# Optimization experiments

Measured on AMD Instinct MI355X. Metric: run time of the kernel, lower is better.

The kernel has to match this reference:

```python
import jax, jax.numpy as jnp
import numpy as np

B, S, IN_DIM, OUT_DIM, HID = 16, 256, 128, 128, 512


def setup_inputs() -> dict:
    key = jax.random.key(0)
    ks = jax.random.split(key, 7)
    x = jax.random.normal(ks[0], (B, S, IN_DIM), dtype=jnp.float32)
    # hypernet linear 1: input_dim -> hyper_hidden_dim
    W1 = jax.random.normal(ks[1], (IN_DIM, HID), dtype=jnp.float32) / np.sqrt(IN_DIM)
    b1 = jax.random.normal(ks[2], (HID,), dtype=jnp.float32) * 0.01
    # hypernet linear 2: hyper_hidden_dim -> input_dim * output_dim
    W2 = jax.random.normal(ks[3], (HID, IN_DIM * OUT_DIM), dtype=jnp.float32) / np.sqrt(HID)
    b2 = jax.random.normal(ks[4], (IN_DIM * OUT_DIM,), dtype=jnp.float32) * 0.01
    # final fc: output_dim -> output_dim
    Wfc = jax.random.normal(ks[5], (OUT_DIM, OUT_DIM), dtype=jnp.float32) / np.sqrt(OUT_DIM)
    bfc = jax.random.normal(ks[6], (OUT_DIM,), dtype=jnp.float32) * 0.01
    return {"x": x, "W1": W1, "b1": b1, "W2": W2, "b2": b2, "Wfc": Wfc, "bfc": bfc}


def reference(x, W1, b1, W2, b2, Wfc, bfc):
    # hypernet: per-token generated weight matrix Wx [B,S,IN,OUT]
    h = jax.nn.relu(jnp.einsum('bsi,ih->bsh', x, W1) + b1)
    Wx = (jnp.einsum('bsh,ho->bso', h, W2) + b2).reshape(x.shape[0], x.shape[1], IN_DIM, OUT_DIM)
    # batched vector-matrix product per (b,s), then sum over s -> [B, OUT]
    y = jnp.einsum('bsi,bsio->bo', x, Wx)
    return y @ Wfc + bfc
```

## Files before the change

kernel.cpp:

```cpp
#include <hip/hip_runtime.h>


typedef __attribute__((ext_vector_type(8))) short     s16x8;
typedef __attribute__((ext_vector_type(8))) unsigned short u16x8;
typedef __attribute__((ext_vector_type(4))) float     f32x4;

__device__ __forceinline__ unsigned short f2bf(float f) {
    union { float f; unsigned int u; } v; v.f = f;
    unsigned int r = v.u + 0x7FFFu + ((v.u >> 16) & 1u);
    return (unsigned short)(r >> 16);
}
__device__ __forceinline__ float bf2f(unsigned short u) {
    union { unsigned int u; float f; } v; v.u = ((unsigned int)u) << 16;
    return v.f;
}

#define OFF_MP   0
#define OFF_PART 2097152
#define OFF_SXP  3145728

__global__ __launch_bounds__(256) void k_AB(const float* __restrict__ x,
        const float* __restrict__ W1, const float* __restrict__ b1,
        float* __restrict__ Mp, float* __restrict__ sxp) {
    __shared__ __align__(16) unsigned char smem[87296];
    auto Ws  = (unsigned short (*)[136])(smem);
    auto xA  = (unsigned short (*)[136])(smem + 17408);
    auto xTl = (unsigned short (*)[136])(smem + 52224);
    auto Wt  = (float (*)[33])(smem + 52224);
    float* b1s = (float*)(smem + 87040);
    auto hts = (unsigned short (*)[136])(smem);

    const int tid = threadIdx.x;
    const int b  = blockIdx.x >> 4;
    const int hb = (blockIdx.x >> 1) & 7;
    const int sh = blockIdx.x & 1;

    {
        const int r = tid >> 1, q = tid & 1;
        const float* xrow = &x[(size_t)(b * 256 + sh * 128 + r) * 128 + q * 64];
        #pragma unroll
        for (int m = 0; m < 8; ++m) {
            const float4 v0 = *(const float4*)&xrow[m * 8];
            const float4 v1 = *(const float4*)&xrow[m * 8 + 4];
            unsigned short t8[8] __attribute__((aligned(16))) = {
                f2bf(v0.x), f2bf(v0.y), f2bf(v0.z), f2bf(v0.w),
                f2bf(v1.x), f2bf(v1.y), f2bf(v1.z), f2bf(v1.w)};
            *(u16x8*)&xA[r][q * 64 + m * 8] = *(u16x8*)t8;
        }
        if (tid < 64) b1s[tid] = b1[hb * 64 + tid];
    }
    for (int hq = 0; hq < 2; ++hq) {
        __syncthreads();
        #pragma unroll
        for (int p = 0; p < 16; ++p) {
            const int flat = p * 256 + tid;
            const int i = flat >> 5, hc = flat & 31;
            Wt[i][hc] = W1[(size_t)i * 512 + hb * 64 + hq * 32 + hc];
        }
        __syncthreads();
        {
            const int h2 = tid >> 3, pt = tid & 7;
            unsigned short t16[16] __attribute__((aligned(16)));
            #pragma unroll
            for (int m = 0; m < 16; ++m)
                t16[m] = f2bf(Wt[pt * 16 + m][h2]);
            *(u16x8*)&Ws[hq * 32 + h2][pt * 16]     = *(u16x8*)&t16[0];
            *(u16x8*)&Ws[hq * 32 + h2][pt * 16 + 8] = *(u16x8*)&t16[8];
        }
    }
    __syncthreads();

    const int w = tid >> 6, lane = tid & 63;
    const int wr = w >> 1, wc = w & 1;
    const int l15 = lane & 15, kl = lane >> 4;
    f32x4 zero = {0.f, 0.f, 0.f, 0.f};

    f32x4 acc[4][2];
    #pragma unroll
    for (int i = 0; i < 4; ++i)
        #pragma unroll
        for (int j = 0; j < 2; ++j) acc[i][j] = zero;
    #pragma unroll
    for (int ks = 0; ks < 4; ++ks) {
        s16x8 a[4], bb[2];
        #pragma unroll
        for (int f = 0; f < 4; ++f)
            a[f] = *(const s16x8*)&xA[wr * 64 + f * 16 + l15][ks * 32 + kl * 8];
        #pragma unroll
        for (int f = 0; f < 2; ++f)
            bb[f] = *(const s16x8*)&Ws[wc * 32 + f * 16 + l15][ks * 32 + kl * 8];
        #pragma unroll
        for (int fr = 0; fr < 4; ++fr)
            #pragma unroll
            for (int fc = 0; fc < 2; ++fc)
                acc[fr][fc] = __builtin_amdgcn_mfma_f32_16x16x32_bf16(a[fr], bb[fc], acc[fr][fc], 0, 0, 0);
    }
    __syncthreads();

    {
        const int i = tid >> 1, q = tid & 1;
        float sacc = 0.f;
        unsigned short t64[64] __attribute__((aligned(16)));
        #pragma unroll
        for (int m = 0; m < 64; ++m) {
            const unsigned short u = xA[q * 64 + m][i];
            sacc += bf2f(u);
            t64[m] = u;
        }
        #pragma unroll
        for (int v = 0; v < 8; ++v)
            *(u16x8*)&xTl[i][q * 64 + v * 8] = *(u16x8*)&t64[v * 8];
        if (hb == 0)
            sxp[(size_t)((sh * 2 + q) * 16 + b) * 128 + i] = sacc;
    }
    __syncthreads();

    #pragma unroll
    for (int fr = 0; fr < 4; ++fr)
        #pragma unroll
        for (int fc = 0; fc < 2; ++fc)
            #pragma unroll
            for (int j = 0; j < 4; ++j) {
                const int tok = wr * 64 + fr * 16 + kl * 4 + j;
                const int hid = wc * 32 + fc * 16 + l15;
                const float v = acc[fr][fc][j] + b1s[hid];
                hts[hid][tok] = f2bf(v > 0.f ? v : 0.f);
            }
    __syncthreads();

    f32x4 acc2[2][4];
    #pragma unroll
    for (int i = 0; i < 2; ++i)
        #pragma unroll
        for (int j = 0; j < 4; ++j) acc2[i][j] = zero;
    #pragma unroll
    for (int ks = 0; ks < 4; ++ks) {
        s16x8 a2[2], b2f[4];
        #pragma unroll
        for (int f = 0; f < 2; ++f)
            a2[f] = *(const s16x8*)&hts[wr * 32 + f * 16 + l15][ks * 32 + kl * 8];
        #pragma unroll
        for (int f = 0; f < 4; ++f)
            b2f[f] = *(const s16x8*)&xTl[wc * 64 + f * 16 + l15][ks * 32 + kl * 8];
        #pragma unroll
        for (int fr = 0; fr < 2; ++fr)
            #pragma unroll
            for (int fc = 0; fc < 4; ++fc)
                acc2[fr][fc] = __builtin_amdgcn_mfma_f32_16x16x32_bf16(a2[fr], b2f[fc], acc2[fr][fc], 0, 0, 0);
    }
    const size_t mpbase = (size_t)(sh * 16 + b) * 65536;
    #pragma unroll
    for (int fr = 0; fr < 2; ++fr)
        #pragma unroll
        for (int fc = 0; fc < 4; ++fc)
            #pragma unroll
            for (int j = 0; j < 4; ++j) {
                const int h = hb * 64 + wr * 32 + fr * 16 + kl * 4 + j;
                const int i = wc * 64 + fc * 16 + l15;
                Mp[mpbase + (size_t)h * 128 + i] = acc2[fr][fc][j];
            }
}

__global__ __launch_bounds__(256) void k_C(const float* __restrict__ Mp,
        const float* __restrict__ W2, float* __restrict__ part) {
    __shared__ float Ms[16][128];
    const int tid = threadIdx.x;
    const int p = blockIdx.x;
    const int k0 = p * 128;
    #pragma unroll
    for (int r = 0; r < 8; ++r) {
        const int flat = r * 256 + tid;
        const int b = flat >> 7, kk = flat & 127;
        Ms[b][kk] = Mp[(size_t)b * 65536 + k0 + kk]
                  + Mp[(size_t)(16 + b) * 65536 + k0 + kk];
    }
    __syncthreads();
    const int o4 = (tid & 31) * 4;
    const int g  = tid >> 5;
    float4 a0 = {0.f, 0.f, 0.f, 0.f}, a1 = a0;
    #pragma unroll 8
    for (int kk = 0; kk < 128; ++kk) {
        const float4 wv = *(const float4*)&W2[(size_t)(k0 + kk) * 128 + o4];
        const float m0 = Ms[g * 2][kk], m1 = Ms[g * 2 + 1][kk];
        a0.x += m0 * wv.x; a0.y += m0 * wv.y; a0.z += m0 * wv.z; a0.w += m0 * wv.w;
        a1.x += m1 * wv.x; a1.y += m1 * wv.y; a1.z += m1 * wv.z; a1.w += m1 * wv.w;
    }
    *(float4*)&part[(size_t)(p * 16 + g * 2) * 128 + o4]     = a0;
    *(float4*)&part[(size_t)(p * 16 + g * 2 + 1) * 128 + o4] = a1;
}

__global__ __launch_bounds__(1024) void k_D(const float* __restrict__ part,
        const float* __restrict__ sxp, const float* __restrict__ b2,
        const float* __restrict__ Wfc, const float* __restrict__ bfc,
        float* __restrict__ out) {
    __shared__ float sh[8][128];
    __shared__ float sxs[128];
    __shared__ float ysum[128];
    __shared__ float ysh[128];
    const int b = blockIdx.x;
    const int t = threadIdx.x & 127;
    const int g = threadIdx.x >> 7;
    float y = 0.f;
    #pragma unroll 8
    for (int pp = g * 64; pp < g * 64 + 64; ++pp)
        y += part[(size_t)(pp * 16 + b) * 128 + t];
    sh[g][t] = y;
    __syncthreads();
    if (g == 0) {
        float yy = sh[0][t];
        #pragma unroll
        for (int j = 1; j < 8; ++j) yy += sh[j][t];
        ysum[t] = yy;
        sxs[t] = sxp[(size_t)(0 * 16 + b) * 128 + t] + sxp[(size_t)(1 * 16 + b) * 128 + t]
               + sxp[(size_t)(2 * 16 + b) * 128 + t] + sxp[(size_t)(3 * 16 + b) * 128 + t];
    }
    __syncthreads();
    float yb = 0.f;
    #pragma unroll
    for (int i = g * 16; i < g * 16 + 16; ++i)
        yb += sxs[i] * b2[i * 128 + t];
    sh[g][t] = yb;
    __syncthreads();
    if (g == 0) {
        float yy = ysum[t];
        #pragma unroll
        for (int j = 0; j < 8; ++j) yy += sh[j][t];
        ysh[t] = yy;
    }
    __syncthreads();
    float f = 0.f;
    #pragma unroll
    for (int oo = g * 16; oo < g * 16 + 16; ++oo)
        f += ysh[oo] * Wfc[oo * 128 + t];
    sh[g][t] = f;
    __syncthreads();
    if (g == 0) {
        float s = bfc[t];
        #pragma unroll
        for (int j = 0; j < 8; ++j) s += sh[j][t];
        out[b * 128 + t] = s;
    }
}

extern "C" void kernel_launch(void* const* d_in, const int* in_sizes, int n_in,
                              void* d_out, int out_size, void* d_ws, size_t ws_size,
                              hipStream_t stream) {
    const float* x   = (const float*)d_in[0];
    const float* W1  = (const float*)d_in[1];
    const float* b1  = (const float*)d_in[2];
    const float* W2  = (const float*)d_in[3];
    const float* b2  = (const float*)d_in[4];
    const float* Wfc = (const float*)d_in[5];
    const float* bfc = (const float*)d_in[6];
    float* ws  = (float*)d_ws;
    float* Mp   = ws + OFF_MP;
    float* part = ws + OFF_PART;
    float* sxp  = ws + OFF_SXP;
    float* out  = (float*)d_out;

    k_AB<<<256, 256, 0, stream>>>(x, W1, b1, Mp, sxp);
    k_C <<<512, 256, 0, stream>>>(Mp, W2, part);
    k_D <<<16, 1024, 0, stream>>>(part, sxp, b2, Wfc, bfc, out);
}
```

Before: 34.70 us.

## Fuse final reduction kernel into k_C via atomic completion counter

Merges the last two kernels into one. Every block of the 512-block GEMV kernel bumps a global counter when it finishes, and the first 16 blocks spin until all 512 are done before running the per-batch reduction and the final fc. This removes one kernel launch and its gap, but the tail now runs on 256 threads instead of 1024. It also relies on all 512 blocks being resident or progressing while 16 blocks spin, which risks deadlock or an early timeout exit that would give wrong results.

```diff
diff --git a/kernel.cpp b/kernel.cpp
--- a/kernel.cpp
+++ b/kernel.cpp
@@ -18,10 +18,12 @@
 #define OFF_MP   0
 #define OFF_PART 2097152
 #define OFF_SXP  3145728
+#define OFF_CNT  3153920
 
 __global__ __launch_bounds__(256) void k_AB(const float* __restrict__ x,
         const float* __restrict__ W1, const float* __restrict__ b1,
-        float* __restrict__ Mp, float* __restrict__ sxp) {
+        float* __restrict__ Mp, float* __restrict__ sxp,
+        unsigned int* __restrict__ cnt) {
     __shared__ __align__(16) unsigned char smem[87296];
     auto Ws  = (unsigned short (*)[136])(smem);
     auto xA  = (unsigned short (*)[136])(smem + 17408);
@@ -35,6 +37,9 @@
     const int hb = (blockIdx.x >> 1) & 7;
     const int sh = blockIdx.x & 1;
 
+    if (blockIdx.x == 0 && tid == 0)
+        __hip_atomic_store(cnt, 0u, __ATOMIC_RELAXED, __HIP_MEMORY_SCOPE_AGENT);
+
     {
         const int r = tid >> 1, q = tid & 1;
         const float* xrow = &x[(size_t)(b * 256 + sh * 128 + r) * 128 + q * 64];
@@ -161,84 +166,90 @@
             }
 }
 
-__global__ __launch_bounds__(256) void k_C(const float* __restrict__ Mp,
-        const float* __restrict__ W2, float* __restrict__ part) {
+__global__ __launch_bounds__(256) void k_CD(const float* __restrict__ Mp,
+        const float* __restrict__ W2, const float* __restrict__ sxp,
+        const float* __restrict__ b2, const float* __restrict__ Wfc,
+        const float* __restrict__ bfc, float* __restrict__ part,
+        float* __restrict__ out, unsigned int* __restrict__ cnt) {
     __shared__ float Ms[16][128];
-    const int tid = threadIdx.x;
-    const int p = blockIdx.x;
-    const int k0 = p * 128;
-    #pragma unroll
-    for (int r = 0; r < 8; ++r) {
-        const int flat = r * 256 + tid;
-        const int b = flat >> 7, kk = flat & 127;
-        Ms[b][kk] = Mp[(size_t)b * 65536 + k0 + kk]
-                  + Mp[(size_t)(16 + b) * 65536 + k0 + kk];
-    }
-    __syncthreads();
-    const int o4 = (tid & 31) * 4;
-    const int g  = tid >> 5;
-    float4 a0 = {0.f, 0.f, 0.f, 0.f}, a1 = a0;
-    #pragma unroll 8
-    for (int kk = 0; kk < 128; ++kk) {
-        const float4 wv = *(const float4*)&W2[(size_t)(k0 + kk) * 128 + o4];
-        const float m0 = Ms[g * 2][kk], m1 = Ms[g * 2 + 1][kk];
-        a0.x += m0 * wv.x; a0.y += m0 * wv.y; a0.z += m0 * wv.z; a0.w += m0 * wv.w;
-        a1.x += m1 * wv.x; a1.y += m1 * wv.y; a1.z += m1 * wv.z; a1.w += m1 * wv.w;
-    }
-    *(float4*)&part[(size_t)(p * 16 + g * 2) * 128 + o4]     = a0;
-    *(float4*)&part[(size_t)(p * 16 + g * 2 + 1) * 128 + o4] = a1;
-}
-
-__global__ __launch_bounds__(1024) void k_D(const float* __restrict__ part,
-        const float* __restrict__ sxp, const float* __restrict__ b2,
-        const float* __restrict__ Wfc, const float* __restrict__ bfc,
-        float* __restrict__ out) {
-    __shared__ float sh[8][128];
+    __shared__ float sh2[2][128];
     __shared__ float sxs[128];
     __shared__ float ysum[128];
     __shared__ float ysh[128];
-    const int b = blockIdx.x;
-    const int t = threadIdx.x & 127;
-    const int g = threadIdx.x >> 7;
-    float y = 0.f;
-    #pragma unroll 8
-    for (int pp = g * 64; pp < g * 64 + 64; ++pp)
-        y += part[(size_t)(pp * 16 + b) * 128 + t];
-    sh[g][t] = y;
-    __syncthreads();
-    if (g == 0) {
-        float yy = sh[0][t];
-        #pragma unroll
-        for (int j = 1; j < 8; ++j) yy += sh[j][t];
-        ysum[t] = yy;
-        sxs[t] = sxp[(size_t)(0 * 16 + b) * 128 + t] + sxp[(size_t)(1 * 16 + b) * 128 + t]
-               + sxp[(size_t)(2 * 16 + b) * 128 + t] + sxp[(size_t)(3 * 16 + b) * 128 + t];
-    }
-    __syncthreads();
-    float yb = 0.f;
-    #pragma unroll
-    for (int i = g * 16; i < g * 16 + 16; ++i)
-        yb += sxs[i] * b2[i * 128 + t];
-    sh[g][t] = yb;
-    __syncthreads();
-    if (g == 0) {
-        float yy = ysum[t];
-        #pragma unroll
-        for (int j = 0; j < 8; ++j) yy += sh[j][t];
-        ysh[t] = yy;
-    }
-    __syncthreads();
-    float f = 0.f;
-    #pragma unroll
-    for (int oo = g * 16; oo < g * 16 + 16; ++oo)
-        f += ysh[oo] * Wfc[oo * 128 + t];
-    sh[g][t] = f;
-    __syncthreads();
-    if (g == 0) {
-        float s = bfc[t];
-        #pragma unroll
-        for (int j = 0; j < 8; ++j) s += sh[j][t];
-        out[b * 128 + t] = s;
+    const int tid = threadIdx.x;
+    const int p = blockIdx.x;
+
+    {
+        const int k0 = p * 128;
+        #pragma unroll
+        for (int r = 0; r < 8; ++r) {
+            const int flat = r * 256 + tid;
+            const int b = flat >> 7, kk = flat & 127;
+            Ms[b][kk] = Mp[(size_t)b * 65536 + k0 + kk]
+                      + Mp[(size_t)(16 + b) * 65536 + k0 + kk];
+        }
+        __syncthreads();
+        const int o4 = (tid & 31) * 4;
+        const int g  = tid >> 5;
+        float4 a0 = {0.f, 0.f, 0.f, 0.f}, a1 = a0;
+        #pragma unroll 8
+        for (int kk = 0; kk < 128; ++kk) {
+            const float4 wv = *(const float4*)&W2[(size_t)(k0 + kk) * 128 + o4];
+            const float m0 = Ms[g * 2][kk], m1 = Ms[g * 2 + 1][kk];
+            a0.x += m0 * wv.x; a0.y += m0 * wv.y; a0.z += m0 * wv.z; a0.w += m0 * wv.w;
+            a1.x += m1 * wv.x; a1.y += m1 * wv.y; a1.z += m1 * wv.z; a1.w += m1 * wv.w;
+        }
+        *(float4*)&part[(size_t)(p * 16 + g * 2) * 128 + o4]     = a0;
+        *(float4*)&part[(size_t)(p * 16 + g * 2 + 1) * 128 + o4] = a1;
+    }
+
+    __syncthreads();
+    if (tid == 0) {
+        __threadfence();
+        __hip_atomic_fetch_add(cnt, 1u, __ATOMIC_ACQ_REL, __HIP_MEMORY_SCOPE_AGENT);
+    }
+    if (p >= 16) return;
+    if (tid == 0) {
+        long spins = 0;
+        while (__hip_atomic_load(cnt, __ATOMIC_ACQUIRE, __HIP_MEMORY_SCOPE_AGENT) < 512u) {
+            __builtin_amdgcn_s_sleep(2);
+            if (++spins > (1L << 26)) break;
+        }
+    }
+    __syncthreads();
+
+    {
+        const int b = p;
+        const int t = tid & 127;
+        const int g = tid >> 7;
+        float y = 0.f;
+        #pragma unroll 8
+        for (int pp = g * 256; pp < g * 256 + 256; ++pp)
+            y += part[(size_t)(pp * 16 + b) * 128 + t];
+        sh2[g][t] = y;
+        __syncthreads();
+        if (g == 0) {
+            ysum[t] = sh2[0][t] + sh2[1][t];
+            sxs[t] = sxp[(size_t)(0 * 16 + b) * 128 + t] + sxp[(size_t)(1 * 16 + b) * 128 + t]
+                   + sxp[(size_t)(2 * 16 + b) * 128 + t] + sxp[(size_t)(3 * 16 + b) * 128 + t];
+        }
+        __syncthreads();
+        float yb = 0.f;
+        #pragma unroll 8
+        for (int i = g * 64; i < g * 64 + 64; ++i)
+            yb += sxs[i] * b2[i * 128 + t];
+        sh2[g][t] = yb;
+        __syncthreads();
+        if (g == 0) ysh[t] = ysum[t] + sh2[0][t] + sh2[1][t];
+        __syncthreads();
+        float f = 0.f;
+        #pragma unroll 8
+        for (int oo = g * 64; oo < g * 64 + 64; ++oo)
+            f += ysh[oo] * Wfc[oo * 128 + t];
+        sh2[g][t] = f;
+        __syncthreads();
+        if (g == 0)
+            out[b * 128 + t] = bfc[t] + sh2[0][t] + sh2[1][t];
     }
 }
 
@@ -256,9 +267,9 @@
     float* Mp   = ws + OFF_MP;
     float* part = ws + OFF_PART;
     float* sxp  = ws + OFF_SXP;
+    unsigned int* cnt = (unsigned int*)(ws + OFF_CNT);
     float* out  = (float*)d_out;
 
-    k_AB<<<256, 256, 0, stream>>>(x, W1, b1, Mp, sxp);
-    k_C <<<512, 256, 0, stream>>>(Mp, W2, part);
-    k_D <<<16, 1024, 0, stream>>>(part, sxp, b2, Wfc, bfc, out);
-}
+    k_AB<<<256, 256, 0, stream>>>(x, W1, b1, Mp, sxp, cnt);
+    k_CD<<<512, 256, 0, stream>>>(Mp, W2, sxp, b2, Wfc, bfc, part, out, cnt);
+}
```

After: 71.97 us. 107% more time.
